# Kernel optimization log

Measured on AMD Instinct MI355X. Metric: run time of the kernel, lower is better.

The kernel has to match this reference:

```python
import jax, jax.numpy as jnp
import numpy as np

N_NODES = 50000
N_EDGES = 800000
IN_DIM = 128
HID_DIM = 128
N_CLASSES = 40


def setup_inputs() -> dict:
    key = jax.random.key(0)
    ks = jax.random.split(key, 12)
    s = 0.05
    inp = {
        "X": jax.random.normal(ks[0], (N_NODES, IN_DIM), jnp.float32),
        "A": jax.random.randint(ks[1], (2, N_EDGES), 0, N_NODES, dtype=jnp.int64),
        "W0": jax.random.normal(ks[2], (HID_DIM, IN_DIM), jnp.float32) * s,
        "b0": jnp.zeros((HID_DIM,), jnp.float32),
        "W1": jax.random.normal(ks[3], (HID_DIM, HID_DIM), jnp.float32) * s,
        "b1": jnp.zeros((HID_DIM,), jnp.float32),
        "W2": jax.random.normal(ks[4], (HID_DIM, HID_DIM), jnp.float32) * s,
        "b2": jnp.zeros((HID_DIM,), jnp.float32),
        "W3": jax.random.normal(ks[5], (HID_DIM, HID_DIM), jnp.float32) * s,
        "b3": jnp.zeros((HID_DIM,), jnp.float32),
        "Wf": jax.random.normal(ks[6], (N_CLASSES, HID_DIM), jnp.float32) * s,
        "bf": jnp.zeros((N_CLASSES,), jnp.float32),
    }
    return inp


def _gcn_conv(x, W, b, src, dst):
    # FrobeniusNormGCNConv: normalize weight by Frobenius norm, then standard GCNConv
    Wn = W / jnp.linalg.norm(W)
    h = x @ Wn.T  # [N, out]
    # gcn_norm with self-loops (edge weight 1.0): deg over targets + 1 self loop
    ones = jnp.ones((dst.shape[0],), h.dtype)
    deg = jax.ops.segment_sum(ones, dst, num_segments=N_NODES) + 1.0
    dinv = jax.lax.rsqrt(deg)  # [N]
    norm = dinv[src] * dinv[dst]  # [E]
    # scatter-add of normalized source messages into targets
    agg = jax.ops.segment_sum(norm[:, None] * h[src], dst, num_segments=N_NODES)
    # self-loop contribution: dinv[i]^2 * h[i]; bias added after aggregation
    return agg + (dinv * dinv)[:, None] * h + b


def reference(X, A, W0, b0, W1, b1, W2, b2, W3, b3, Wf, bf):
    src, dst = A[0], A[1]
    h = _gcn_conv(X, W0, b0, src, dst)
    skip = h
    for W, b in ((W1, b1), (W2, b2), (W3, b3)):
        h = _gcn_conv(h, W, b, src, dst)
        h = jax.nn.relu(h)
        h = h + skip  # residual skip (dropout identity in eval mode)
        skip = h
    return h @ Wf.T + bf
```

## Files before the change

kernel.cpp:

```cpp
#include <hip/hip_runtime.h>

#define N_NODES_C 50000
#define N_EDGES_C 800000
#define DIM 128
#define NCLS 40
#define NBUK 32
#define BCAP 32768
#define NOCT 16
#define SLAB 57344
#define ZROW N_NODES_C

typedef __attribute__((ext_vector_type(8))) short bf16x8;
typedef __attribute__((ext_vector_type(4))) float f32x4;

__device__ inline float bf2f(unsigned short u) {
    union { unsigned int i; float f; } c;
    c.i = ((unsigned int)u) << 16;
    return c.f;
}
__device__ inline unsigned short f2bf(float f) {
    union { float f; unsigned int i; } c;
    c.f = f;
    unsigned int x = c.i;
    x += 0x7fffu + ((x >> 16) & 1u);
    return (unsigned short)(x >> 16);
}
__device__ inline void unp8(const uint4& g, float* f) {
    f[0] = __uint_as_float(g.x << 16); f[1] = __uint_as_float(g.x & 0xFFFF0000u);
    f[2] = __uint_as_float(g.y << 16); f[3] = __uint_as_float(g.y & 0xFFFF0000u);
    f[4] = __uint_as_float(g.z << 16); f[5] = __uint_as_float(g.z & 0xFFFF0000u);
    f[6] = __uint_as_float(g.w << 16); f[7] = __uint_as_float(g.w & 0xFFFF0000u);
}

__global__ __launch_bounds__(256) void k_pre(const float* __restrict__ W0,
                                             const float* __restrict__ W1,
                                             const float* __restrict__ W2,
                                             const float* __restrict__ W3,
                                             const float* __restrict__ Wf,
                                             unsigned short* __restrict__ Wb,
                                             unsigned short* __restrict__ Wfb,
                                             float* __restrict__ scale_inv,
                                             int* __restrict__ gcount,
                                             unsigned short* __restrict__ Gb) {
    int b = blockIdx.x;
    if (b < 64) {
        int m = b >> 4;
        int idx = (b & 15) * 256 + threadIdx.x;
        const float* W = m == 0 ? W0 : m == 1 ? W1 : m == 2 ? W2 : W3;
        float4 v = reinterpret_cast<const float4*>(W)[idx];
        reinterpret_cast<ushort4*>(Wb + (size_t)m * DIM * DIM)[idx] =
            make_ushort4(f2bf(v.x), f2bf(v.y), f2bf(v.z), f2bf(v.w));
        return;
    }
    b -= 64;
    if (b < 5) {
        int idx = b * 256 + threadIdx.x;
        float4 v = reinterpret_cast<const float4*>(Wf)[idx];
        reinterpret_cast<ushort4*>(Wfb)[idx] =
            make_ushort4(f2bf(v.x), f2bf(v.y), f2bf(v.z), f2bf(v.w));
        return;
    }
    b -= 5;
    if (b == 4) {
        if (threadIdx.x < DIM / 4)
            reinterpret_cast<ushort4*>(Gb + (size_t)ZROW * DIM)[threadIdx.x] =
                make_ushort4(0, 0, 0, 0);
        return;
    }
    if (b == 0 && threadIdx.x < NBUK) gcount[threadIdx.x] = 0;
    const float* W = b == 0 ? W0 : b == 1 ? W1 : b == 2 ? W2 : W3;
    float s = 0.f;
    for (int i = threadIdx.x; i < DIM * DIM; i += 256) {
        float v = W[i];
        s += v * v;
    }
    #pragma unroll
    for (int off = 32; off >= 1; off >>= 1) s += __shfl_down(s, off);
    __shared__ float red[4];
    int lane = threadIdx.x & 63, wid = threadIdx.x >> 6;
    if (lane == 0) red[wid] = s;
    __syncthreads();
    if (threadIdx.x == 0) {
        float tot = red[0] + red[1] + red[2] + red[3];
        scale_inv[b] = 1.0f / sqrtf(tot);
    }
}

__global__ __launch_bounds__(256) void k_bucket(const int* __restrict__ A,
                                                int* __restrict__ gcount,
                                                unsigned int* __restrict__ ebuk, int E) {
    __shared__ int cnt[NBUK];
    __shared__ int gbase[NBUK];
    int tid = threadIdx.x;
    if (tid < NBUK) cnt[tid] = 0;
    __syncthreads();
    int e0 = blockIdx.x * 1024;
    int s[4], d[4], b[4], r[4];
    #pragma unroll
    for (int j = 0; j < 4; ++j) {
        int e = e0 + j * 256 + tid;
        if (e < E) {
            s[j] = A[e];
            d[j] = A[E + e];
            b[j] = (int)(((unsigned long long)(unsigned)d[j] * NBUK) / N_NODES_C);
            r[j] = atomicAdd(&cnt[b[j]], 1);
        } else {
            b[j] = -1;
        }
    }
    __syncthreads();
    if (tid < NBUK) gbase[tid] = atomicAdd(&gcount[tid], cnt[tid]);
    __syncthreads();
    #pragma unroll
    for (int j = 0; j < 4; ++j) {
        if (b[j] >= 0) {
            int pos = gbase[b[j]] + r[j];
            if (pos < BCAP)
                ebuk[(size_t)b[j] * BCAP + pos] =
                    ((unsigned)d[j] << 16) | (unsigned)s[j];
        }
    }
}

__global__ __launch_bounds__(512) void k_csr(const unsigned int* __restrict__ ebuk,
                                             const int* __restrict__ gcount,
                                             int* __restrict__ ptr,
                                             float* __restrict__ dinv,
                                             unsigned short* __restrict__ esrc) {
    __shared__ unsigned int dlo[NOCT / 2][1568];
    __shared__ int wsum2[8], wpre2[8];
    int k = blockIdx.x;
    int tid = threadIdx.x;
    int base = (k * N_NODES_C + NBUK - 1) / NBUK;
    int next = ((k + 1) * N_NODES_C + NBUK - 1) / NBUK;
    int sz = next - base;

    for (int i = tid; i < (NOCT / 2) * 1568; i += 512) (&dlo[0][0])[i] = 0;
    __syncthreads();

    int count = min(gcount[k], BCAP);
    int bucket_base = k * SLAB;
    const unsigned int* eb = ebuk + (size_t)k * BCAP;

    for (int i = tid; i < count; i += 512) {
        unsigned v = eb[i];
        int d = (int)(v >> 16) - base;
        int src = (int)(v & 0xFFFFu);
        int oct = (src * NOCT) / N_NODES_C;
        atomicAdd(&dlo[oct >> 1][d], 1u << ((oct & 1) * 16));
    }
    __syncthreads();

    int degloc[4], degp[4];
    int mysum = 0;
    #pragma unroll
    for (int c = 0; c < 4; ++c) {
        int i = tid * 4 + c;
        int ds = 0;
        if (i < sz) {
            #pragma unroll
            for (int p = 0; p < NOCT / 2; ++p) {
                unsigned v = dlo[p][i];
                ds += (int)(v & 0xFFFFu) + (int)(v >> 16);
            }
        }
        degloc[c] = ds;
        degp[c] = (i < sz) ? ((ds + 15) & ~15) : 0;
        mysum += degp[c];
    }
    int lane = tid & 63, wid = tid >> 6;
    int sc = mysum;
    #pragma unroll
    for (int off = 1; off < 64; off <<= 1) {
        int t = __shfl_up(sc, off);
        if (lane >= off) sc += t;
    }
    if (lane == 63) wsum2[wid] = sc;
    __syncthreads();
    if (tid == 0) {
        int a = 0;
        #pragma unroll
        for (int w = 0; w < 8; ++w) { wpre2[w] = a; a += wsum2[w]; }
    }
    __syncthreads();
    int run = wpre2[wid] + sc - mysum;
    #pragma unroll
    for (int c = 0; c < 4; ++c) {
        int i = tid * 4 + c;
        if (i < sz) {
            ptr[base + i] = ((bucket_base + run) << 8) | (degp[c] >> 4);
            dinv[base + i] = rsqrtf((float)degloc[c] + 1.0f);
            int r = run;
            #pragma unroll
            for (int p = 0; p < NOCT / 2; ++p) {
                unsigned v = dlo[p][i];
                int lo = (int)(v & 0xFFFFu), hi = (int)(v >> 16);
                dlo[p][i] = (unsigned)r | ((unsigned)(r + lo) << 16);
                r += lo + hi;
            }
            for (int j = degloc[c]; j < degp[c]; ++j)
                esrc[bucket_base + run + j] = (unsigned short)ZROW;
            run += degp[c];
        }
    }
    __syncthreads();

    for (int i = tid; i < count; i += 512) {
        unsigned v = eb[i];
        int d = (int)(v >> 16) - base;
        int src = (int)(v & 0xFFFFu);
        int oct = (src * NOCT) / N_NODES_C;
        unsigned old = atomicAdd(&dlo[oct >> 1][d], 1u << ((oct & 1) * 16));
        int pos = (int)((old >> ((oct & 1) * 16)) & 0xFFFFu);
        esrc[bucket_base + pos] = (unsigned short)src;
    }
}

template <bool F32A>
__global__ __launch_bounds__(256) void k_gemm_mfma(const void* __restrict__ Xp,
                                                   const unsigned short* __restrict__ Wb,
                                                   const float* __restrict__ scale_ptr,
                                                   const float* __restrict__ dinv,
                                                   unsigned short* __restrict__ Gb, int N) {
    int tid = threadIdx.x;
    int w = tid >> 6;
    int l = tid & 63;
    int l15 = l & 15;
    int lg = l >> 4;
    int arow = blockIdx.x * 64 + w * 16 + l15;
    if (arow >= N) arow = N - 1;
    float scale = scale_ptr[0];

    f32x4 acc[8];
    #pragma unroll
    for (int ct = 0; ct < 8; ++ct) acc[ct] = f32x4{0.f, 0.f, 0.f, 0.f};

    #pragma unroll
    for (int kc = 0; kc < 4; ++kc) {
        int ko = kc * 32 + lg * 8;
        bf16x8 a;
        if (F32A) {
            const float4* xf = reinterpret_cast<const float4*>(
                (const float*)Xp + (size_t)arow * DIM + ko);
            float4 u = xf[0], v = xf[1];
            a[0] = (short)f2bf(u.x); a[1] = (short)f2bf(u.y);
            a[2] = (short)f2bf(u.z); a[3] = (short)f2bf(u.w);
            a[4] = (short)f2bf(v.x); a[5] = (short)f2bf(v.y);
            a[6] = (short)f2bf(v.z); a[7] = (short)f2bf(v.w);
        } else {
            a = *reinterpret_cast<const bf16x8*>(
                (const unsigned short*)Xp + (size_t)arow * DIM + ko);
        }
        #pragma unroll
        for (int ct = 0; ct < 8; ++ct) {
            bf16x8 b = *reinterpret_cast<const bf16x8*>(&Wb[(size_t)(ct * 16 + l15) * DIM + ko]);
            acc[ct] = __builtin_amdgcn_mfma_f32_16x16x32_bf16(a, b, acc[ct], 0, 0, 0);
        }
    }
    int outrow0 = blockIdx.x * 64 + w * 16 + lg * 4;
    #pragma unroll
    for (int r = 0; r < 4; ++r) {
        int row = outrow0 + r;
        if (row < N) {
            float dv = dinv[row] * scale;
            #pragma unroll
            for (int ct = 0; ct < 8; ++ct)
                Gb[(size_t)row * DIM + ct * 16 + l15] = f2bf(acc[ct][r] * dv);
        }
    }
}

template <bool RELU>
__global__ __launch_bounds__(256) void k_agg(const unsigned short* __restrict__ Gb,
                                             const float* __restrict__ bias,
                                             const float* __restrict__ dinv,
                                             const int* __restrict__ ptr,
                                             const unsigned short* __restrict__ esrc,
                                             const unsigned short* __restrict__ skipb,
                                             unsigned short* __restrict__ outb) {
    int orig = blockIdx.x;
    int xcd = orig & 7;
    int idx = orig >> 3;
    int wgid = (xcd < 4 ? xcd * 1563 : 4 * 1563 + (xcd - 4) * 1562) + idx;

    int n = wgid * 4 + (threadIdx.x >> 6);
    int l = threadIdx.x & 63;
    int grp = l >> 4, li = l & 15;
    const uint4* __restrict__ Gv = reinterpret_cast<const uint4*>(Gb);
    int p = ptr[n];
    int beg = p >> 8;
    int niter = p & 255;

    uint4 gu = Gv[(size_t)n * 16 + li];
    uint4 su;
    if (RELU) su = reinterpret_cast<const uint4*>(skipb)[(size_t)n * 16 + li];
    const float4* b4p = reinterpret_cast<const float4*>(bias);
    float4 ba = b4p[li * 2], bb = b4p[li * 2 + 1];
    float di = dinv[n];

    float acc[8] = {};
    float t[8];
    for (int it = 0; it < niter; ++it) {
        int e = beg + it * 16;
        int s0 = esrc[e + grp];
        int s1 = esrc[e + 4 + grp];
        int s2 = esrc[e + 8 + grp];
        int s3 = esrc[e + 12 + grp];
        uint4 g0 = Gv[(size_t)s0 * 16 + li];
        uint4 g1 = Gv[(size_t)s1 * 16 + li];
        uint4 g2 = Gv[(size_t)s2 * 16 + li];
        uint4 g3 = Gv[(size_t)s3 * 16 + li];
        unp8(g0, t);
        #pragma unroll
        for (int j = 0; j < 8; ++j) acc[j] += t[j];
        unp8(g1, t);
        #pragma unroll
        for (int j = 0; j < 8; ++j) acc[j] += t[j];
        unp8(g2, t);
        #pragma unroll
        for (int j = 0; j < 8; ++j) acc[j] += t[j];
        unp8(g3, t);
        #pragma unroll
        for (int j = 0; j < 8; ++j) acc[j] += t[j];
    }
    #pragma unroll
    for (int j = 0; j < 8; ++j) {
        acc[j] += __shfl_xor(acc[j], 16);
        acc[j] += __shfl_xor(acc[j], 32);
    }
    if (grp == 0) {
        float gs[8];
        unp8(gu, gs);
        float bv[8] = {ba.x, ba.y, ba.z, ba.w, bb.x, bb.y, bb.z, bb.w};
        float v[8];
        #pragma unroll
        for (int j = 0; j < 8; ++j) v[j] = fmaf(di, acc[j] + gs[j], bv[j]);
        if (RELU) {
            float ss[8];
            unp8(su, ss);
            #pragma unroll
            for (int j = 0; j < 8; ++j) v[j] = fmaxf(v[j], 0.f) + ss[j];
        }
        uint4 o;
        o.x = (unsigned)f2bf(v[0]) | ((unsigned)f2bf(v[1]) << 16);
        o.y = (unsigned)f2bf(v[2]) | ((unsigned)f2bf(v[3]) << 16);
        o.z = (unsigned)f2bf(v[4]) | ((unsigned)f2bf(v[5]) << 16);
        o.w = (unsigned)f2bf(v[6]) | ((unsigned)f2bf(v[7]) << 16);
        reinterpret_cast<uint4*>(outb)[(size_t)n * 16 + li] = o;
    }
}

__global__ __launch_bounds__(256) void k_final(const unsigned short* __restrict__ Hb,
                                               const unsigned short* __restrict__ Wfb,
                                               const float* __restrict__ bf,
                                               float* __restrict__ out, int N) {
    int tid = threadIdx.x;
    int w = tid >> 6;
    int l = tid & 63;
    int l15 = l & 15;
    int lg = l >> 4;
    int arow = blockIdx.x * 64 + w * 16 + l15;
    if (arow >= N) arow = N - 1;

    f32x4 acc[3];
    #pragma unroll
    for (int ct = 0; ct < 3; ++ct) acc[ct] = f32x4{0.f, 0.f, 0.f, 0.f};

    #pragma unroll
    for (int kc = 0; kc < 4; ++kc) {
        int ko = kc * 32 + lg * 8;
        bf16x8 a = *reinterpret_cast<const bf16x8*>(&Hb[(size_t)arow * DIM + ko]);
        #pragma unroll
        for (int ct = 0; ct < 3; ++ct) {
            int wr = ct * 16 + l15;
            if (wr >= NCLS) wr = 0;
            bf16x8 b = *reinterpret_cast<const bf16x8*>(&Wfb[(size_t)wr * DIM + ko]);
            acc[ct] = __builtin_amdgcn_mfma_f32_16x16x32_bf16(a, b, acc[ct], 0, 0, 0);
        }
    }
    int outrow0 = blockIdx.x * 64 + w * 16 + lg * 4;
    #pragma unroll
    for (int ct = 0; ct < 3; ++ct) {
        int c = ct * 16 + l15;
        if (c < NCLS) {
            float bias = bf[c];
            #pragma unroll
            for (int r = 0; r < 4; ++r) {
                int row = outrow0 + r;
                if (row < N) out[(size_t)row * NCLS + c] = acc[ct][r] + bias;
            }
        }
    }
}

extern "C" void kernel_launch(void* const* d_in, const int* in_sizes, int n_in,
                              void* d_out, int out_size, void* d_ws, size_t ws_size,
                              hipStream_t stream) {
    (void)in_sizes; (void)n_in; (void)out_size; (void)ws_size;
    const float* X  = (const float*)d_in[0];
    const int*   A  = (const int*)d_in[1];
    const float* W0 = (const float*)d_in[2];
    const float* b0 = (const float*)d_in[3];
    const float* W1 = (const float*)d_in[4];
    const float* b1 = (const float*)d_in[5];
    const float* W2 = (const float*)d_in[6];
    const float* b2 = (const float*)d_in[7];
    const float* W3 = (const float*)d_in[8];
    const float* b3 = (const float*)d_in[9];
    const float* Wf = (const float*)d_in[10];
    const float* bf = (const float*)d_in[11];
    float* out = (float*)d_out;

    char* base_ws = (char*)d_ws;
    size_t off = 0;
    auto alloc = [&](size_t bytes) -> char* {
        char* p = base_ws + off;
        off = (off + bytes + 255) & ~(size_t)255;
        return p;
    };
    float* scale_inv = (float*)alloc(4 * sizeof(float));
    int*   ptr    = (int*)alloc(N_NODES_C * sizeof(int));
    float* dinv   = (float*)alloc(N_NODES_C * sizeof(float));
    int*   gcount = (int*)alloc(NBUK * sizeof(int));
    unsigned int*   ebuk = (unsigned int*)alloc((size_t)NBUK * BCAP * sizeof(unsigned int));
    unsigned short* esrc = (unsigned short*)alloc((size_t)NBUK * SLAB * sizeof(unsigned short));
    unsigned short* Gb  = (unsigned short*)alloc((size_t)(N_NODES_C + 1) * DIM * sizeof(unsigned short));
    unsigned short* Hb1 = (unsigned short*)alloc((size_t)N_NODES_C * DIM * sizeof(unsigned short));
    unsigned short* Hb2 = (unsigned short*)alloc((size_t)N_NODES_C * DIM * sizeof(unsigned short));
    unsigned short* Wb  = (unsigned short*)alloc((size_t)4 * DIM * DIM * sizeof(unsigned short));
    unsigned short* Wfb = (unsigned short*)alloc((size_t)NCLS * DIM * sizeof(unsigned short));

    k_pre<<<74, 256, 0, stream>>>(W0, W1, W2, W3, Wf, Wb, Wfb, scale_inv, gcount, Gb);
    k_bucket<<<(N_EDGES_C + 1023) / 1024, 256, 0, stream>>>(A, gcount, ebuk, N_EDGES_C);
    k_csr<<<NBUK, 512, 0, stream>>>(ebuk, gcount, ptr, dinv, esrc);

    const int gemm_grid = (N_NODES_C + 63) / 64;
    const int agg_grid  = N_NODES_C / 4;

    k_gemm_mfma<true><<<gemm_grid, 256, 0, stream>>>(X, Wb + 0 * DIM * DIM, scale_inv + 0, dinv, Gb, N_NODES_C);
    k_agg<false><<<agg_grid, 256, 0, stream>>>(Gb, b0, dinv, ptr, esrc, nullptr, Hb1);
    k_gemm_mfma<false><<<gemm_grid, 256, 0, stream>>>(Hb1, Wb + 1 * DIM * DIM, scale_inv + 1, dinv, Gb, N_NODES_C);
    k_agg<true><<<agg_grid, 256, 0, stream>>>(Gb, b1, dinv, ptr, esrc, Hb1, Hb2);
    k_gemm_mfma<false><<<gemm_grid, 256, 0, stream>>>(Hb2, Wb + 2 * DIM * DIM, scale_inv + 2, dinv, Gb, N_NODES_C);
    k_agg<true><<<agg_grid, 256, 0, stream>>>(Gb, b2, dinv, ptr, esrc, Hb2, Hb1);
    k_gemm_mfma<false><<<gemm_grid, 256, 0, stream>>>(Hb1, Wb + 3 * DIM * DIM, scale_inv + 3, dinv, Gb, N_NODES_C);
    k_agg<true><<<agg_grid, 256, 0, stream>>>(Gb, b3, dinv, ptr, esrc, Hb1, Hb2);
    k_final<<<(N_NODES_C + 63) / 64, 256, 0, stream>>>(Hb2, Wfb, bf, out, N_NODES_C);
}
```

Baseline: 293.5 us.

## Fuse GEMM and aggregation layers into one cooperative persistent kernel

Replaces the nine per-layer GEMM/aggregation/final launches with a single cooperative persistent kernel that loops over tiles and uses grid-wide syncs between stages. This removes kernel launch gaps and tail drain between stages. It drops the XCD-aware block remapping in aggregation and adds grid.sync costs. Occupancy may be capped by the launch bounds. If the cooperative launch fails, it falls back to separate launches.

Result: slower. 925.0 us (+215.1%).

```diff
diff --git a/kernel.cpp b/kernel.cpp
--- a/kernel.cpp
+++ b/kernel.cpp
@@ -1,4 +1,7 @@
 #include <hip/hip_runtime.h>
+#include <hip/hip_cooperative_groups.h>
+
+namespace cg = cooperative_groups;
 
 #define N_NODES_C 50000
 #define N_EDGES_C 800000
@@ -9,6 +12,8 @@
 #define NOCT 16
 #define SLAB 57344
 #define ZROW N_NODES_C
+#define GEMM_TILES ((N_NODES_C + 63) / 64)
+#define AGG_WGS (N_NODES_C / 4)
 
 typedef __attribute__((ext_vector_type(8))) short bf16x8;
 typedef __attribute__((ext_vector_type(4))) float f32x4;
@@ -217,19 +222,17 @@
 }
 
 template <bool F32A>
-__global__ __launch_bounds__(256) void k_gemm_mfma(const void* __restrict__ Xp,
-                                                   const unsigned short* __restrict__ Wb,
-                                                   const float* __restrict__ scale_ptr,
-                                                   const float* __restrict__ dinv,
-                                                   unsigned short* __restrict__ Gb, int N) {
+__device__ inline void gemm_tile(int tile, const void* __restrict__ Xp,
+                                 const unsigned short* __restrict__ Wb,
+                                 float scale, const float* __restrict__ dinv,
+                                 unsigned short* __restrict__ Gb) {
     int tid = threadIdx.x;
     int w = tid >> 6;
     int l = tid & 63;
     int l15 = l & 15;
     int lg = l >> 4;
-    int arow = blockIdx.x * 64 + w * 16 + l15;
-    if (arow >= N) arow = N - 1;
-    float scale = scale_ptr[0];
+    int arow = tile * 64 + w * 16 + l15;
+    if (arow >= N_NODES_C) arow = N_NODES_C - 1;
 
     f32x4 acc[8];
     #pragma unroll
@@ -257,11 +260,11 @@
             acc[ct] = __builtin_amdgcn_mfma_f32_16x16x32_bf16(a, b, acc[ct], 0, 0, 0);
         }
     }
-    int outrow0 = blockIdx.x * 64 + w * 16 + lg * 4;
+    int outrow0 = tile * 64 + w * 16 + lg * 4;
     #pragma unroll
     for (int r = 0; r < 4; ++r) {
         int row = outrow0 + r;
-        if (row < N) {
+        if (row < N_NODES_C) {
             float dv = dinv[row] * scale;
             #pragma unroll
             for (int ct = 0; ct < 8; ++ct)
@@ -271,19 +274,14 @@
 }
 
 template <bool RELU>
-__global__ __launch_bounds__(256) void k_agg(const unsigned short* __restrict__ Gb,
-                                             const float* __restrict__ bias,
-                                             const float* __restrict__ dinv,
-                                             const int* __restrict__ ptr,
-                                             const unsigned short* __restrict__ esrc,
-                                             const unsigned short* __restrict__ skipb,
-                                             unsigned short* __restrict__ outb) {
-    int orig = blockIdx.x;
-    int xcd = orig & 7;
-    int idx = orig >> 3;
-    int wgid = (xcd < 4 ? xcd * 1563 : 4 * 1563 + (xcd - 4) * 1562) + idx;
-
-    int n = wgid * 4 + (threadIdx.x >> 6);
+__device__ inline void agg_tile(int wg, const unsigned short* __restrict__ Gb,
+                                const float* __restrict__ bias,
+                                const float* __restrict__ dinv,
+                                const int* __restrict__ ptr,
+                                const unsigned short* __restrict__ esrc,
+                                const unsigned short* __restrict__ skipb,
+                                unsigned short* __restrict__ outb) {
+    int n = wg * 4 + (threadIdx.x >> 6);
     int l = threadIdx.x & 63;
     int grp = l >> 4, li = l & 15;
     const uint4* __restrict__ Gv = reinterpret_cast<const uint4*>(Gb);
@@ -350,17 +348,17 @@
     }
 }
 
-__global__ __launch_bounds__(256) void k_final(const unsigned short* __restrict__ Hb,
-                                               const unsigned short* __restrict__ Wfb,
-                                               const float* __restrict__ bf,
-                                               float* __restrict__ out, int N) {
+__device__ inline void final_tile(int tile, const unsigned short* __restrict__ Hb,
+                                  const unsigned short* __restrict__ Wfb,
+                                  const float* __restrict__ bf,
+                                  float* __restrict__ out) {
     int tid = threadIdx.x;
     int w = tid >> 6;
     int l = tid & 63;
     int l15 = l & 15;
     int lg = l >> 4;
-    int arow = blockIdx.x * 64 + w * 16 + l15;
-    if (arow >= N) arow = N - 1;
+    int arow = tile * 64 + w * 16 + l15;
+    if (arow >= N_NODES_C) arow = N_NODES_C - 1;
 
     f32x4 acc[3];
     #pragma unroll
@@ -378,7 +376,7 @@
             acc[ct] = __builtin_amdgcn_mfma_f32_16x16x32_bf16(a, b, acc[ct], 0, 0, 0);
         }
     }
-    int outrow0 = blockIdx.x * 64 + w * 16 + lg * 4;
+    int outrow0 = tile * 64 + w * 16 + lg * 4;
     #pragma unroll
     for (int ct = 0; ct < 3; ++ct) {
         int c = ct * 16 + l15;
@@ -387,10 +385,77 @@
             #pragma unroll
             for (int r = 0; r < 4; ++r) {
                 int row = outrow0 + r;
-                if (row < N) out[(size_t)row * NCLS + c] = acc[ct][r] + bias;
+                if (row < N_NODES_C) out[(size_t)row * NCLS + c] = acc[ct][r] + bias;
             }
         }
     }
+}
+
+__global__ __launch_bounds__(256, 4) void k_mega(const float* __restrict__ X,
+                                                 const unsigned short* __restrict__ Wb,
+                                                 const unsigned short* __restrict__ Wfb,
+                                                 const float* __restrict__ scale_inv,
+                                                 const float* __restrict__ dinv,
+                                                 const int* __restrict__ ptr,
+                                                 const unsigned short* __restrict__ esrc,
+                                                 const float* __restrict__ b0,
+                                                 const float* __restrict__ b1,
+                                                 const float* __restrict__ b2,
+                                                 const float* __restrict__ b3,
+                                                 const float* __restrict__ bf,
+                                                 unsigned short* __restrict__ Gb,
+                                                 unsigned short* __restrict__ Hb1,
+                                                 unsigned short* __restrict__ Hb2,
+                                                 float* __restrict__ out) {
+    cg::grid_group grid = cg::this_grid();
+    const int nblk = (int)gridDim.x;
+
+    for (int t = blockIdx.x; t < GEMM_TILES; t += nblk)
+        gemm_tile<true>(t, X, Wb, scale_inv[0], dinv, Gb);
+    grid.sync();
+    for (int wg = blockIdx.x; wg < AGG_WGS; wg += nblk)
+        agg_tile<false>(wg, Gb, b0, dinv, ptr, esrc, nullptr, Hb1);
+    grid.sync();
+    for (int t = blockIdx.x; t < GEMM_TILES; t += nblk)
+        gemm_tile<false>(t, Hb1, Wb + 1 * DIM * DIM, scale_inv[1], dinv, Gb);
+    grid.sync();
+    for (int wg = blockIdx.x; wg < AGG_WGS; wg += nblk)
+        agg_tile<true>(wg, Gb, b1, dinv, ptr, esrc, Hb1, Hb2);
+    grid.sync();
+    for (int t = blockIdx.x; t < GEMM_TILES; t += nblk)
+        gemm_tile<false>(t, Hb2, Wb + 2 * DIM * DIM, scale_inv[2], dinv, Gb);
+    grid.sync();
+    for (int wg = blockIdx.x; wg < AGG_WGS; wg += nblk)
+        agg_tile<true>(wg, Gb, b2, dinv, ptr, esrc, Hb2, Hb1);
+    grid.sync();
+    for (int t = blockIdx.x; t < GEMM_TILES; t += nblk)
+        gemm_tile<false>(t, Hb1, Wb + 3 * DIM * DIM, scale_inv[3], dinv, Gb);
+    grid.sync();
+    for (int wg = blockIdx.x; wg < AGG_WGS; wg += nblk)
+        agg_tile<true>(wg, Gb, b3, dinv, ptr, esrc, Hb1, Hb2);
+    grid.sync();
+    for (int t = blockIdx.x; t < GEMM_TILES; t += nblk)
+        final_tile(t, Hb2, Wfb, bf, out);
+}
+
+template <bool F32A>
+__global__ __launch_bounds__(256) void k_gemm_w(const void* Xp, const unsigned short* Wb,
+                                                const float* sp, const float* dinv,
+                                                unsigned short* Gb) {
+    gemm_tile<F32A>(blockIdx.x, Xp, Wb, sp[0], dinv, Gb);
+}
+template <bool RELU>
+__global__ __launch_bounds__(256) void k_agg_w(const unsigned short* Gb, const float* bias,
+                                               const float* dinv, const int* ptr,
+                                               const unsigned short* esrc,
+                                               const unsigned short* skipb,
+                                               unsigned short* outb) {
+    agg_tile<RELU>(blockIdx.x, Gb, bias, dinv, ptr, esrc, skipb, outb);
+}
+__global__ __launch_bounds__(256) void k_final_w(const unsigned short* Hb,
+                                                 const unsigned short* Wfb,
+                                                 const float* bf, float* out) {
+    final_tile(blockIdx.x, Hb, Wfb, bf, out);
 }
 
 extern "C" void kernel_launch(void* const* d_in, const int* in_sizes, int n_in,
@@ -434,16 +499,37 @@
     k_bucket<<<(N_EDGES_C + 1023) / 1024, 256, 0, stream>>>(A, gcount, ebuk, N_EDGES_C);
     k_csr<<<NBUK, 512, 0, stream>>>(ebuk, gcount, ptr, dinv, esrc);
 
-    const int gemm_grid = (N_NODES_C + 63) / 64;
-    const int agg_grid  = N_NODES_C / 4;
-
-    k_gemm_mfma<true><<<gemm_grid, 256, 0, stream>>>(X, Wb + 0 * DIM * DIM, scale_inv + 0, dinv, Gb, N_NODES_C);
-    k_agg<false><<<agg_grid, 256, 0, stream>>>(Gb, b0, dinv, ptr, esrc, nullptr, Hb1);
-    k_gemm_mfma<false><<<gemm_grid, 256, 0, stream>>>(Hb1, Wb + 1 * DIM * DIM, scale_inv + 1, dinv, Gb, N_NODES_C);
-    k_agg<true><<<agg_grid, 256, 0, stream>>>(Gb, b1, dinv, ptr, esrc, Hb1, Hb2);
-    k_gemm_mfma<false><<<gemm_grid, 256, 0, stream>>>(Hb2, Wb + 2 * DIM * DIM, scale_inv + 2, dinv, Gb, N_NODES_C);
-    k_agg<true><<<agg_grid, 256, 0, stream>>>(Gb, b2, dinv, ptr, esrc, Hb2, Hb1);
-    k_gemm_mfma<false><<<gemm_grid, 256, 0, stream>>>(Hb1, Wb + 3 * DIM * DIM, scale_inv + 3, dinv, Gb, N_NODES_C);
-    k_agg<true><<<agg_grid, 256, 0, stream>>>(Gb, b3, dinv, ptr, esrc, Hb1, Hb2);
-    k_final<<<(N_NODES_C + 63) / 64, 256, 0, stream>>>(Hb2, Wfb, bf, out, N_NODES_C);
-}
+    int maxb = 0;
+    if (hipOccupancyMaxActiveBlocksPerMultiprocessor(
+            &maxb, reinterpret_cast<const void*>(k_mega), 256, 0) != hipSuccess || maxb < 1)
+        maxb = 1;
+    int nblk = maxb * 256;
+    if (nblk > 2048) nblk = 2048;
+
+    const void* Xv = (const void*)X;
+    const void* Hb1v = (const void*)Hb1;
+    const void* Hb2v = (const void*)Hb2;
+    void* kargs[] = {
+        (void*)&X, (void*)&Wb, (void*)&Wfb, (void*)&scale_inv, (void*)&dinv,
+        (void*)&ptr, (void*)&esrc, (void*)&b0, (void*)&b1, (void*)&b2, (void*)&b3,
+        (void*)&bf, (void*)&Gb, (void*)&Hb1, (void*)&Hb2, (void*)&out
+    };
+    hipError_t rc = hipLaunchCooperativeKernel(
+        reinterpret_cast<const void*>(k_mega), dim3(nblk), dim3(256), kargs, 0, stream);
+
+    if (rc != hipSuccess) {
+        const float* si0 = scale_inv + 0;
+        const float* si1 = scale_inv + 1;
+        const float* si2 = scale_inv + 2;
+        const float* si3 = scale_inv + 3;
+        k_gemm_w<true><<<GEMM_TILES, 256, 0, stream>>>(Xv, Wb, si0, dinv, Gb);
+        k_agg_w<false><<<AGG_WGS, 256, 0, stream>>>(Gb, b0, dinv, ptr, esrc, nullptr, Hb1);
+        k_gemm_w<false><<<GEMM_TILES, 256, 0, stream>>>(Hb1v, Wb + 1 * DIM * DIM, si1, dinv, Gb);
+        k_agg_w<true><<<AGG_WGS, 256, 0, stream>>>(Gb, b1, dinv, ptr, esrc, Hb1, Hb2);
+        k_gemm_w<false><<<GEMM_TILES, 256, 0, stream>>>(Hb2v, Wb + 2 * DIM * DIM, si2, dinv, Gb);
+        k_agg_w<true><<<AGG_WGS, 256, 0, stream>>>(Gb, b2, dinv, ptr, esrc, Hb2, Hb1);
+        k_gemm_w<false><<<GEMM_TILES, 256, 0, stream>>>(Hb1v, Wb + 3 * DIM * DIM, si3, dinv, Gb);
+        k_agg_w<true><<<AGG_WGS, 256, 0, stream>>>(Gb, b3, dinv, ptr, esrc, Hb1, Hb2);
+        k_final_w<<<GEMM_TILES, 256, 0, stream>>>(Hb2, Wfb, bf, out);
+    }
+}
```
